# Optimization experiments

Measured on AMD Instinct MI355X. Metric: run time of the kernel, lower is better.

The kernel has to match this reference:

```python
import jax, jax.numpy as jnp
import numpy as np

N, E, D, H, OUT, L, AH = 50000, 800000, 128, 128, 2, 4, 16
LN_EPS = 1e-5


def setup_inputs() -> dict:
    key = jax.random.key(0)
    ks = jax.random.split(key, 8)
    s = lambda k, shape, scale: jax.random.normal(k, shape, jnp.float32) * scale
    return {
        "node_features": jax.random.normal(ks[0], (N, D), jnp.float32),
        "edge_index": jax.random.randint(ks[1], (2, E), 0, N),
        "W_self": s(ks[2], (L, D, H), 0.05),
        "b_self": jnp.zeros((L, H), jnp.float32),
        "W_ctx": s(ks[3], (L, 2 * D, H), 0.05),
        "b_ctx": jnp.zeros((L, H), jnp.float32),
        "att_W1": s(ks[4], (L, H, AH), 0.1),
        "att_b1": jnp.zeros((L, AH), jnp.float32),
        "att_w2": s(ks[5], (L, AH), 0.1),
        "ln_gamma": jnp.ones((L, H), jnp.float32),
        "ln_beta": jnp.zeros((L, H), jnp.float32),
        "fusion_logits": jnp.ones((L,), jnp.float32),
        "cls_W": s(ks[6], (H, OUT), 0.05),
        "cls_b": jnp.zeros((OUT,), jnp.float32),
    }


def _aggregate(x, src, tgt, n):
    # PyG add-aggregation of message cat([x_i - x_j, x_j]) at target nodes.
    # sum_over_edges(x_tgt - x_src) at tgt == deg(tgt)*x[tgt] - sum x_src, so we
    # avoid materializing the [E, 2D] edge tensor.
    ones = jnp.ones((src.shape[0],), x.dtype)
    deg = jax.ops.segment_sum(ones, tgt, num_segments=n)          # [N]
    agg_j = jax.ops.segment_sum(x[src], tgt, num_segments=n)      # [N, D]
    return jnp.concatenate([deg[:, None] * x - agg_j, agg_j], -1)  # [N, 2D]


def _layer_norm(x, gamma, beta):
    mu = x.mean(axis=-1, keepdims=True)
    var = ((x - mu) ** 2).mean(axis=-1, keepdims=True)
    return (x - mu) * jax.lax.rsqrt(var + LN_EPS) * gamma + beta


def _conv(x, src, tgt, Ws, bs, Wc, bc, A1, a1b, a2):
    n = x.shape[0]
    self_view = x @ Ws + bs                              # [N, H]
    out_view = _aggregate(x, src, tgt, n) @ Wc + bc      # outgoing (edge_index)
    in_view = _aggregate(x, tgt, src, n) @ Wc + bc       # incoming (reversed)
    mv = jnp.stack([self_view, out_view, in_view], axis=1)  # [N, 3, H]
    scores = jnp.einsum('nvh,ha->nva', jnp.tanh(jnp.einsum('nvh,ha->nva', mv, A1) + a1b), a2[:, None])[..., 0]
    w = jax.nn.softmax(scores, axis=1)                    # softmax over 3 views
    return jnp.einsum('nv,nvh->nh', w, mv)


def reference(node_features, edge_index, W_self, b_self, W_ctx, b_ctx,
              att_W1, att_b1, att_w2, ln_gamma, ln_beta,
              fusion_logits, cls_W, cls_b):
    src, tgt = edge_index[0], edge_index[1]
    x = node_features
    layer_outputs = []
    for l in range(L):
        h = _conv(x, src, tgt, W_self[l], b_self[l], W_ctx[l], b_ctx[l],
                  att_W1[l], att_b1[l], att_w2[l])
        h = jax.nn.relu(_layer_norm(h, ln_gamma[l], ln_beta[l]))
        # dropout is identity in eval mode
        x = h + x if l > 0 else h
        layer_outputs.append(x)
    fw = jax.nn.softmax(fusion_logits)
    fused = sum(fw[i] * layer_outputs[i] for i in range(L))
    return fused @ cls_W + cls_b
```

## Files before the change

### kernel.cpp

```cpp
#include <hip/hip_runtime.h>

#define N_NODES 50000
#define N_EDGES 800000
#define DD 128
#define HH 128
#define LL 4
#define AHH 16
#define LN_EPS 1e-5f
#define NCOLS 432
#define SCAN_B 512
#define SCAN_NB ((N_NODES + SCAN_B - 1) / SCAN_B)
#define WTPAD 136
#define WT_BLOCKS ((LL*NCOLS*DD)/256)
#define NBKT 196
#define BKT_CAP 8192
#define CVT_BLOCKS ((N_NODES*DD + 255)/256)
#define BKT_BLOCKS ((N_EDGES + 2047)/2048)

typedef unsigned short u16;
typedef unsigned int u32;
typedef __attribute__((ext_vector_type(8))) short short8;
typedef __attribute__((ext_vector_type(4))) float f32x4;

__device__ __forceinline__ float bf2f(u16 h){
  u32 u = ((u32)h) << 16;
  return __builtin_bit_cast(float, u);
}
__device__ __forceinline__ float bflo(u32 v){ return __builtin_bit_cast(float, v << 16); }
__device__ __forceinline__ float bfhi(u32 v){ return __builtin_bit_cast(float, v & 0xffff0000u); }
__device__ __forceinline__ u16 f2bf(float x){
  u32 u = __builtin_bit_cast(u32, x);
  u += 0x7fffu + ((u >> 16) & 1u);
  return (u16)(u >> 16);
}

__global__ void k_fail(float* out){
  int i = blockIdx.x*256 + threadIdx.x;
  if (i < N_NODES*2) out[i] = 1.0e6f;
}

__global__ __launch_bounds__(256) void k_cvt_hist_bkt(const float* __restrict__ X,
    u16* __restrict__ Xb, const int* __restrict__ ei, int* degO, int* degI,
    int* gcur, u32* __restrict__ bktO, u32* __restrict__ bktI){
  if (blockIdx.x < CVT_BLOCKS){
    int i = blockIdx.x*256 + threadIdx.x;
    if (i < N_NODES*DD) Xb[i] = f2bf(X[i]);
    if (i < N_EDGES){
      atomicAdd(&degO[ei[N_EDGES + i]], 1);
      atomicAdd(&degI[ei[i]], 1);
    }
    return;
  }
  __shared__ int histO[NBKT], histI[NBKT], baseO[NBKT], baseI[NBKT];
  int tid = threadIdx.x;
  int e0 = (blockIdx.x - CVT_BLOCKS)*2048;
  if (tid < NBKT){ histO[tid] = 0; histI[tid] = 0; }
  __syncthreads();
  int s[8], t[8];
  #pragma unroll
  for (int k = 0; k < 8; ++k){
    int e = e0 + k*256 + tid;
    bool ok = e < N_EDGES;
    s[k] = ok ? ei[e] : -1;
    t[k] = ok ? ei[N_EDGES + e] : -1;
    if (ok){
      atomicAdd(&histO[t[k] >> 8], 1);
      atomicAdd(&histI[s[k] >> 8], 1);
    }
  }
  __syncthreads();
  if (tid < NBKT){
    baseO[tid] = atomicAdd(&gcur[tid],        histO[tid]);
    baseI[tid] = atomicAdd(&gcur[NBKT + tid], histI[tid]);
  }
  __syncthreads();
  if (tid < NBKT){ histO[tid] = 0; histI[tid] = 0; }
  __syncthreads();
  #pragma unroll
  for (int k = 0; k < 8; ++k){
    if (s[k] >= 0){
      int bO = t[k] >> 8, bI = s[k] >> 8;
      int rO = atomicAdd(&histO[bO], 1);
      int rI = atomicAdd(&histI[bI], 1);
      u32 iO = (u32)bO*BKT_CAP + (u32)(baseO[bO] + rO);
      u32 iI = (u32)bI*BKT_CAP + (u32)(baseI[bI] + rI);
      if (iO >= (u32)NBKT*BKT_CAP) iO = (u32)NBKT*BKT_CAP - 1;
      if (iI >= (u32)NBKT*BKT_CAP) iI = (u32)NBKT*BKT_CAP - 1;
      bktO[iO] = ((u32)(t[k] & 255) << 16) | (u32)s[k];
      bktI[iI] = ((u32)(s[k] & 255) << 16) | (u32)t[k];
    }
  }
}

__global__ __launch_bounds__(SCAN_B) void k_scan1(const int* __restrict__ degO,
                                                  const int* __restrict__ degI, int* bsum){
  int b = blockIdx.x, t = threadIdx.x;
  const int* deg = blockIdx.y ? degI : degO;
  int i = b*SCAN_B + t;
  int v = (i < N_NODES) ? deg[i] : 0;
  #pragma unroll
  for (int m = 1; m < 64; m <<= 1) v += __shfl_xor(v, m);
  __shared__ int ws[SCAN_B/64];
  if ((t & 63) == 0) ws[t >> 6] = v;
  __syncthreads();
  if (t == 0){
    int s = 0;
    for (int w = 0; w < SCAN_B/64; ++w) s += ws[w];
    bsum[blockIdx.y*SCAN_NB + b] = s;
  }
}
__global__ void k_scan2(int* bsum, int* offO, int* offI){
  if (threadIdx.x == 0){
    int run = 0;
    for (int i = 0; i < SCAN_NB; ++i){ int v = bsum[i]; bsum[i] = run; run += v; }
    offO[N_NODES] = run;
    run = 0;
    for (int i = 0; i < SCAN_NB; ++i){ int v = bsum[SCAN_NB+i]; bsum[SCAN_NB+i] = run; run += v; }
    offI[N_NODES] = run;
  }
}
__global__ __launch_bounds__(SCAN_B) void k_scan3(const int* __restrict__ degO,
                                                  const int* __restrict__ degI,
                                                  const int* __restrict__ bsum,
                                                  int* offO, int* offI){
  int b = blockIdx.x, t = threadIdx.x, lane = t & 63, w = t >> 6;
  const int* deg = blockIdx.y ? degI : degO;
  int* off = blockIdx.y ? offI : offO;
  int i = b*SCAN_B + t;
  int v = (i < N_NODES) ? deg[i] : 0;
  int x = v;
  #pragma unroll
  for (int m = 1; m < 64; m <<= 1){ int tt = __shfl_up(x, m); if (lane >= m) x += tt; }
  __shared__ int ws[SCAN_B/64];
  if (lane == 63) ws[w] = x;
  __syncthreads();
  int woff = 0;
  for (int k = 0; k < w; ++k) woff += ws[k];
  if (i < N_NODES) off[i] = bsum[blockIdx.y*SCAN_NB + b] + woff + x - v;
}

__global__ __launch_bounds__(256) void k_packsort(const float* __restrict__ Wself,
                       const float* __restrict__ Wctx,
                       const float* __restrict__ A1, const float* __restrict__ bs,
                       const float* __restrict__ bc, u16* __restrict__ WT,
                       float* bsA, float* bcA,
                       const u32* __restrict__ bktO, const u32* __restrict__ bktI,
                       const int* __restrict__ offO, const int* __restrict__ offI,
                       int* __restrict__ csrO, int* __restrict__ csrI){
  if (blockIdx.x > WT_BLOCKS){
    int sb = blockIdx.x - (WT_BLOCKS + 1);
    int d = sb >= NBKT;
    int b = d ? sb - NBKT : sb;
    const u32* bkt = d ? bktI : bktO;
    const int* off = d ? offI : offO;
    int* csr = d ? csrI : csrO;
    __shared__ int hist[256], pref[256], cur[256], wsum[4];
    int tid = threadIdx.x;
    int lo = b*256, hi = min(lo + 256, N_NODES);
    int gbase = off[lo];
    int cnt = off[hi] - gbase;
    if (cnt > BKT_CAP) cnt = BKT_CAP;
    hist[tid] = 0; cur[tid] = 0;
    __syncthreads();
    const u32* bb = bkt + (size_t)b*BKT_CAP;
    for (int i = tid; i < cnt; i += 256) atomicAdd(&hist[bb[i] >> 16], 1);
    __syncthreads();
    {
      int lane = tid & 63, wid = tid >> 6;
      int h = hist[tid], v = h;
      #pragma unroll
      for (int m = 1; m < 64; m <<= 1){ int tt = __shfl_up(v, m); if (lane >= m) v += tt; }
      if (lane == 63) wsum[wid] = v;
      __syncthreads();
      int add = 0;
      for (int w = 0; w < wid; ++w) add += wsum[w];
      pref[tid] = add + v - h;
    }
    __syncthreads();
    for (int i = tid; i < cnt; i += 256){
      u32 ent = bb[i];
      int loc = (int)(ent >> 16);
      int pos = pref[loc] + atomicAdd(&cur[loc], 1);
      csr[gbase + pos] = (int)(ent & 0xffffu);
    }
    return;
  }
  if (blockIdx.x == WT_BLOCKS){
    int i = threadIdx.x;
    if (i < LL*2*AHH){
      int l = i >> 5, which = (i >> 4) & 1, a = i & 15;
      const float* b = which ? (bc + l*HH) : (bs + l*HH);
      const float* A = A1 + (size_t)l*HH*AHH;
      float v = 0.f;
      for (int h = 0; h < HH; ++h) v += b[h] * A[h*AHH + a];
      (which ? bcA : bsA)[l*AHH + a] = v;
    }
    return;
  }
  int idx = blockIdx.x*256 + threadIdx.x;
  int k = idx & 127;
  int j = (idx >> 7) % NCOLS;
  int l = idx / (NCOLS*DD);
  const float* Ws = Wself + (size_t)l*DD*HH;
  const float* Wc = Wctx + (size_t)l*2*DD*HH;
  const float* A  = A1 + (size_t)l*HH*AHH;
  float v = 0.f;
  if (j < 128) v = Ws[k*HH + j];
  else if (j < 256) v = Wc[k*HH + (j-128)];
  else if (j < 384) v = Wc[(128+k)*HH + (j-256)] - Wc[k*HH + (j-256)];
  else if (j < 400){ int a = j-384; for (int h=0; h<HH; ++h) v += Ws[k*HH+h] * A[h*AHH+a]; }
  else if (j < 416){ int a = j-400; for (int h=0; h<HH; ++h) v += Wc[k*HH+h] * A[h*AHH+a]; }
  else { int a = j-416; for (int h=0; h<HH; ++h) v += (Wc[(128+k)*HH+h] - Wc[k*HH+h]) * A[h*AHH+a]; }
  WT[((size_t)l*NCOLS + j)*DD + k] = f2bf(v);
}

struct GemmOut { u16 *S, *P1, *Pd, *SA, *P1A, *PdA; };

__global__ __launch_bounds__(256) void k_gemm(const u16* __restrict__ X,
                                              const u16* __restrict__ WT, GemmOut o){
  __shared__ u16 lw[3*16*WTPAD];
  int tid = threadIdx.x;
  int wid = tid >> 6, lane = tid & 63;
  int m0 = (blockIdx.x*4 + wid)*16;
  bool mvalid = (m0 < N_NODES);
  int m0c = mvalid ? m0 : (N_NODES - 16);
  int l15 = lane & 15, quad = lane >> 4;
  int sr = tid >> 4, sp = tid & 15;

  f32x4 acc[27];
  #pragma unroll
  for (int j = 0; j < 27; ++j) acc[j] = (f32x4){0.f,0.f,0.f,0.f};

  const u16* xr = X + (size_t)(m0c + l15)*DD + quad*8;
  short8 a[4];
  #pragma unroll
  for (int ks = 0; ks < 4; ++ks) a[ks] = *(const short8*)(xr + ks*32);

  short8 st[3];
  #pragma unroll
  for (int k = 0; k < 3; ++k)
    st[k] = *(const short8*)(WT + ((size_t)k*16 + sr)*DD + sp*8);

  for (int stage = 0; stage < 9; ++stage){
    int jbase = stage*3;
    __syncthreads();
    #pragma unroll
    for (int k = 0; k < 3; ++k)
      *(short8*)(&lw[(k*16 + sr)*WTPAD + sp*8]) = st[k];
    __syncthreads();
    if (stage < 8){
      #pragma unroll
      for (int k = 0; k < 3; ++k)
        st[k] = *(const short8*)(WT + ((size_t)(jbase+3+k)*16 + sr)*DD + sp*8);
    }
    #pragma unroll
    for (int k = 0; k < 3; ++k){
      const u16* wb = &lw[(k*16 + l15)*WTPAD + quad*8];
      #pragma unroll
      for (int ks = 0; ks < 4; ++ks){
        short8 b = *(const short8*)(wb + ks*32);
        acc[jbase+k] = __builtin_amdgcn_mfma_f32_16x16x32_bf16(a[ks], b, acc[jbase+k], 0, 0, 0);
      }
    }
  }
  if (!mvalid) return;
  #pragma unroll
  for (int j = 0; j < 27; ++j){
    int col = j*16 + l15;
    #pragma unroll
    for (int r = 0; r < 4; ++r){
      int row = m0 + quad*4 + r;
      u16 hv = f2bf(acc[j][r]);
      if (col < 128)      o.S  [(size_t)row*128 + col]        = hv;
      else if (col < 256) o.P1 [(size_t)row*128 + col - 128]  = hv;
      else if (col < 384) o.Pd [(size_t)row*128 + col - 256]  = hv;
      else if (col < 400) o.SA [(size_t)row*16  + col - 384]  = hv;
      else if (col < 416) o.P1A[(size_t)row*16  + col - 400]  = hv;
      else                o.PdA[(size_t)row*16  + col - 416]  = hv;
    }
  }
}

__global__ __launch_bounds__(256) void k_aggepi(int l,
  const u16* __restrict__ S, const u16* __restrict__ P1,
  const u16* __restrict__ Pd, const u16* __restrict__ PdA,
  const u16* __restrict__ SA, const u16* __restrict__ P1A,
  const int* __restrict__ offO, const int* __restrict__ offI,
  const int* __restrict__ csrO, const int* __restrict__ csrI,
  const float* __restrict__ b_self, const float* __restrict__ b_ctx,
  const float* __restrict__ bsA, const float* __restrict__ bcA,
  const float* __restrict__ att_b1, const float* __restrict__ att_w2,
  const float* __restrict__ gamma, const float* __restrict__ beta,
  const float* __restrict__ flog,
  u16* __restrict__ xb16,
  const float* __restrict__ clsW, const float* __restrict__ clsB,
  float* __restrict__ out)
{
  __shared__ float red[4][288];
  int tid = threadIdx.x;
  int n = (blockIdx.x * 256 + tid) >> 6;
  int wid = tid >> 6;
  int lane = tid & 63;
  int q = lane & 15, g = lane >> 4;
  const u16* PdQ  = Pd  + (q << 3);
  const u16* PdAQ = PdA + ((lane & 7) << 1);

  int begO = offO[n], endO = offO[n+1];
  int begI = offI[n], endI = offI[n+1];

  float aO[8] = {0.f,0.f,0.f,0.f,0.f,0.f,0.f,0.f};
  float aI[8] = {0.f,0.f,0.f,0.f,0.f,0.f,0.f,0.f};
  float oa0 = 0.f, oa1 = 0.f, ia0 = 0.f, ia1 = 0.f;

  int eO = begO, eI = begI;

#define GATH(csr, e, ACC, p0, p1) { \
    int r_ = (csr)[(e) + g]; \
    uint4 v_ = *(const uint4*)(PdQ + (((u32)r_) << 7)); \
    u32 pa_ = *(const u32*)(PdAQ + (((u32)r_) << 4)); \
    ACC[0] += bflo(v_.x); ACC[1] += bfhi(v_.x); \
    ACC[2] += bflo(v_.y); ACC[3] += bfhi(v_.y); \
    ACC[4] += bflo(v_.z); ACC[5] += bfhi(v_.z); \
    ACC[6] += bflo(v_.w); ACC[7] += bfhi(v_.w); \
    p0 += bflo(pa_); p1 += bfhi(pa_); }

#define GATHM(csr, e, end, ACC, p0, p1) { \
    int e_ = (e) + g; \
    bool ok_ = e_ < (end); \
    int r_ = (csr)[ok_ ? e_ : (end)-1]; \
    uint4 v_ = *(const uint4*)(PdQ + (((u32)r_) << 7)); \
    u32 pa_ = *(const u32*)(PdAQ + (((u32)r_) << 4)); \
    if (!ok_){ v_.x = 0u; v_.y = 0u; v_.z = 0u; v_.w = 0u; pa_ = 0u; } \
    ACC[0] += bflo(v_.x); ACC[1] += bfhi(v_.x); \
    ACC[2] += bflo(v_.y); ACC[3] += bfhi(v_.y); \
    ACC[4] += bflo(v_.z); ACC[5] += bfhi(v_.z); \
    ACC[6] += bflo(v_.w); ACC[7] += bfhi(v_.w); \
    p0 += bflo(pa_); p1 += bfhi(pa_); }

  for (; eO + 4 <= endO && eI + 4 <= endI; eO += 4, eI += 4){
    GATH(csrO, eO, aO, oa0, oa1);
    GATH(csrI, eI, aI, ia0, ia1);
  }
  for (; eO + 4 <= endO; eO += 4) GATH(csrO, eO, aO, oa0, oa1);
  for (; eI + 4 <= endI; eI += 4) GATH(csrI, eI, aI, ia0, ia1);
  if (eO < endO) GATHM(csrO, eO, endO, aO, oa0, oa1);
  if (eI < endI) GATHM(csrI, eI, endI, aI, ia0, ia1);

#undef GATH
#undef GATHM

  #pragma unroll
  for (int j = 0; j < 8; ++j){
    aO[j] += __shfl_xor(aO[j], 16); aO[j] += __shfl_xor(aO[j], 32);
    aI[j] += __shfl_xor(aI[j], 16); aI[j] += __shfl_xor(aI[j], 32);
  }
  oa0 += __shfl_xor(oa0, 16); oa0 += __shfl_xor(oa0, 32);
  oa1 += __shfl_xor(oa1, 16); oa1 += __shfl_xor(oa1, 32);
  ia0 += __shfl_xor(ia0, 16); ia0 += __shfl_xor(ia0, 32);
  ia1 += __shfl_xor(ia1, 16); ia1 += __shfl_xor(ia1, 32);

  if (g == 0){
    #pragma unroll
    for (int j = 0; j < 8; ++j){
      red[wid][q*8 + j]       = aO[j];
      red[wid][128 + q*8 + j] = aI[j];
    }
    if (q < 8){
      red[wid][256 + q*2]     = oa0;
      red[wid][256 + q*2 + 1] = oa1;
      red[wid][272 + q*2]     = ia0;
      red[wid][272 + q*2 + 1] = ia1;
    }
  }
  int f0 = lane * 2;
  int a16 = lane & 15;
  float ao0 = red[wid][f0],       ao1 = red[wid][f0 + 1];
  float ai0 = red[wid][128 + f0], ai1 = red[wid][128 + f0 + 1];
  float aoa = red[wid][256 + a16];
  float aia = red[wid][272 + a16];

  float dO = (float)(endO - begO), dI = (float)(endI - begI);

  u32 sv = *(const u32*)(S  + (size_t)n*128 + f0);
  u32 pv = *(const u32*)(P1 + (size_t)n*128 + f0);
  float2 bsv = *(const float2*)(b_self + l*128 + f0);
  float2 bcv = *(const float2*)(b_ctx  + l*128 + f0);
  float p10 = bflo(pv), p11 = bfhi(pv);
  float mv00 = bflo(sv) + bsv.x;
  float mv01 = bfhi(sv) + bsv.y;
  float mv10 = dO*p10 + ao0 + bcv.x, mv11 = dO*p11 + ao1 + bcv.y;
  float mv20 = dI*p10 + ai0 + bcv.x, mv21 = dI*p11 + ai1 + bcv.y;

  int a = a16, v = g;
  float u = 0.f;
  if (v < 3){
    float t;
    if (v == 0)      t = bf2f(SA[(size_t)n*16 + a]) + bsA[l*16 + a];
    else if (v == 1) t = dO*bf2f(P1A[(size_t)n*16 + a]) + aoa + bcA[l*16 + a];
    else             t = dI*bf2f(P1A[(size_t)n*16 + a]) + aia + bcA[l*16 + a];
    u = tanhf(t + att_b1[l*16 + a]) * att_w2[l*16 + a];
  }
  u += __shfl_xor(u, 1); u += __shfl_xor(u, 2);
  u += __shfl_xor(u, 4); u += __shfl_xor(u, 8);
  float s0 = __shfl(u, 0), s1 = __shfl(u, 16), s2 = __shfl(u, 32);
  float mx = fmaxf(s0, fmaxf(s1, s2));
  float e0 = __expf(s0-mx), e1 = __expf(s1-mx), e2 = __expf(s2-mx);
  float inv = 1.f / (e0 + e1 + e2);
  float w0 = e0*inv, w1 = e1*inv, w2v = e2*inv;
  float h0 = w0*mv00 + w1*mv10 + w2v*mv20;
  float h1 = w0*mv01 + w1*mv11 + w2v*mv21;

  float sum = h0 + h1, sq = h0*h0 + h1*h1;
  #pragma unroll
  for (int m = 1; m < 64; m <<= 1){ sum += __shfl_xor(sum, m); sq += __shfl_xor(sq, m); }
  float mu = sum * (1.f/128.f);
  float var = sq * (1.f/128.f) - mu*mu;
  float rs = rsqrtf(var + LN_EPS);
  float2 gv = *(const float2*)(gamma + l*128 + f0);
  float2 bv = *(const float2*)(beta  + l*128 + f0);
  float y0 = fmaxf((h0 - mu)*rs*gv.x + bv.x, 0.f);
  float y1 = fmaxf((h1 - mu)*rs*gv.y + bv.y, 0.f);
  float xn0 = y0, xn1 = y1;
  if (l > 0){
    u32 xv = *(const u32*)(xb16 + (size_t)n*128 + f0);
    xn0 += bflo(xv); xn1 += bfhi(xv);
  }
  *(u32*)(xb16 + (size_t)n*128 + f0) = (u32)f2bf(xn0) | ((u32)f2bf(xn1) << 16);

  float g0 = flog[0], g1 = flog[1], g2 = flog[2], g3 = flog[3];
  float gm = fmaxf(fmaxf(g0,g1), fmaxf(g2,g3));
  float q0 = __expf(g0-gm), q1 = __expf(g1-gm), q2 = __expf(g2-gm), q3 = __expf(g3-gm);
  float fwl = (l==0?q0 : l==1?q1 : l==2?q2 : q3) / (q0+q1+q2+q3);

  float4 w = *(const float4*)(clsW + lane*4);
  float o0 = xn0*w.x + xn1*w.z;
  float o1 = xn0*w.y + xn1*w.w;
  #pragma unroll
  for (int m = 1; m < 64; m <<= 1){ o0 += __shfl_xor(o0, m); o1 += __shfl_xor(o1, m); }
  if (lane == 0){
    float2* op = (float2*)(out + (size_t)n*2);
    float2 prev = (l > 0) ? *op : make_float2(0.f, 0.f);
    float r0 = prev.x + fwl*o0, r1 = prev.y + fwl*o1;
    if (l == LL-1){ r0 += clsB[0]; r1 += clsB[1]; }
    *op = make_float2(r0, r1);
  }
}

extern "C" void kernel_launch(void* const* d_in, const int* in_sizes, int n_in,
                              void* d_out, int out_size, void* d_ws, size_t ws_size,
                              hipStream_t stream){
  const float* X0    = (const float*)d_in[0];
  const int*   EI    = (const int*)d_in[1];
  const float* Wself = (const float*)d_in[2];
  const float* bs    = (const float*)d_in[3];
  const float* Wctx  = (const float*)d_in[4];
  const float* bc    = (const float*)d_in[5];
  const float* A1    = (const float*)d_in[6];
  const float* ab1   = (const float*)d_in[7];
  const float* aw2   = (const float*)d_in[8];
  const float* gam   = (const float*)d_in[9];
  const float* bet   = (const float*)d_in[10];
  const float* flog  = (const float*)d_in[11];
  const float* clsW  = (const float*)d_in[12];
  const float* clsB  = (const float*)d_in[13];
  float* out = (float*)d_out;

  char* wsp = (char*)d_ws;
  size_t o = 0;
  auto alloc = [&](size_t b)->char*{ char* p = wsp + o; o = (o + b + 255) & ~(size_t)255; return p; };
  u16*  xb16  = (u16*) alloc((size_t)N_NODES*128*2);
  u16*  S     = (u16*) alloc((size_t)N_NODES*128*2);
  u16*  P1    = (u16*) alloc((size_t)N_NODES*128*2);
  u16*  Pdb   = (u16*) alloc((size_t)N_NODES*128*2);
  u16*  PdAb  = (u16*) alloc((size_t)N_NODES*16*2);
  u16*  SAb   = (u16*) alloc((size_t)N_NODES*16*2);
  u16*  P1A   = (u16*) alloc((size_t)N_NODES*16*2);
  u16*  WT    = (u16*) alloc((size_t)LL*NCOLS*128*2);
  float* bsA  = (float*)alloc(LL*16*4);
  float* bcA  = (float*)alloc(LL*16*4);
  int* bsum   = (int*) alloc((size_t)2*SCAN_NB*4);
  int* degO   = (int*) alloc((size_t)N_NODES*4);
  int* degI   = (int*) alloc((size_t)N_NODES*4);
  int* gcur   = (int*) alloc((size_t)2*NBKT*4);
  int* offO   = (int*) alloc((size_t)(N_NODES+1)*4);
  int* offI   = (int*) alloc((size_t)(N_NODES+1)*4);
  int* csrO   = (int*) alloc((size_t)N_EDGES*4);
  int* csrI   = (int*) alloc((size_t)N_EDGES*4);

  if (ws_size < o){
    k_fail<<<(N_NODES*2+255)/256, 256, 0, stream>>>(out);
    return;
  }

  u32* bktO = (u32*)S;
  u32* bktI = (u32*)P1;

  (void)hipMemsetAsync(degO, 0, (size_t)((char*)offO - (char*)degO), stream);

  k_cvt_hist_bkt<<<CVT_BLOCKS + BKT_BLOCKS, 256, 0, stream>>>(X0, xb16, EI, degO, degI,
                                                              gcur, bktO, bktI);
  k_scan1<<<dim3(SCAN_NB,2), SCAN_B, 0, stream>>>(degO, degI, bsum);
  k_scan2<<<1, 64, 0, stream>>>(bsum, offO, offI);
  k_scan3<<<dim3(SCAN_NB,2), SCAN_B, 0, stream>>>(degO, degI, bsum, offO, offI);
  k_packsort<<<WT_BLOCKS + 1 + 2*NBKT, 256, 0, stream>>>(Wself, Wctx, A1, bs, bc, WT, bsA, bcA,
                                                         bktO, bktI, offO, offI, csrO, csrI);

  GemmOut go{S, P1, Pdb, SAb, P1A, PdAb};
  const int gemm_blocks = ((N_NODES/16) + 3) / 4;
  for (int l = 0; l < LL; ++l){
    k_gemm<<<gemm_blocks, 256, 0, stream>>>(xb16, WT + (size_t)l*NCOLS*128, go);
    k_aggepi<<<N_NODES/4, 256, 0, stream>>>(l, S, P1, Pdb, PdAb, SAb, P1A,
                                            offO, offI, csrO, csrI,
                                            bs, bc, bsA, bcA, ab1, aw2,
                                            gam, bet, flog, xb16,
                                            clsW, clsB, out);
  }
}
```

Baseline: 612.9 us.

## Derive node degrees from bucket histograms instead of global atomics

Removes the per-edge global atomic degree counting from the conversion kernel. Degrees are now computed per bucket with shared-memory histograms over the already-bucketed edges. Block sums for the scan come straight from the bucket counters, so the scan1 pass goes away. The memset shrinks to the bucket counters, and bucket blocks are reordered to launch before the conversion blocks. The cost is one extra pass that reads the bucket arrays.

```diff
diff --git a/kernel.cpp b/kernel.cpp
--- a/kernel.cpp
+++ b/kernel.cpp
@@ -39,21 +39,17 @@
   if (i < N_NODES*2) out[i] = 1.0e6f;
 }
 
-__global__ __launch_bounds__(256) void k_cvt_hist_bkt(const float* __restrict__ X,
-    u16* __restrict__ Xb, const int* __restrict__ ei, int* degO, int* degI,
+__global__ __launch_bounds__(256) void k_cvt_bkt(const float* __restrict__ X,
+    u16* __restrict__ Xb, const int* __restrict__ ei,
     int* gcur, u32* __restrict__ bktO, u32* __restrict__ bktI){
-  if (blockIdx.x < CVT_BLOCKS){
-    int i = blockIdx.x*256 + threadIdx.x;
+  if (blockIdx.x >= BKT_BLOCKS){
+    int i = (blockIdx.x - BKT_BLOCKS)*256 + threadIdx.x;
     if (i < N_NODES*DD) Xb[i] = f2bf(X[i]);
-    if (i < N_EDGES){
-      atomicAdd(&degO[ei[N_EDGES + i]], 1);
-      atomicAdd(&degI[ei[i]], 1);
-    }
     return;
   }
   __shared__ int histO[NBKT], histI[NBKT], baseO[NBKT], baseI[NBKT];
   int tid = threadIdx.x;
-  int e0 = (blockIdx.x - CVT_BLOCKS)*2048;
+  int e0 = blockIdx.x*2048;
   if (tid < NBKT){ histO[tid] = 0; histI[tid] = 0; }
   __syncthreads();
   int s[8], t[8];
@@ -92,30 +88,32 @@
   }
 }
 
-__global__ __launch_bounds__(SCAN_B) void k_scan1(const int* __restrict__ degO,
-                                                  const int* __restrict__ degI, int* bsum){
-  int b = blockIdx.x, t = threadIdx.x;
-  const int* deg = blockIdx.y ? degI : degO;
-  int i = b*SCAN_B + t;
-  int v = (i < N_NODES) ? deg[i] : 0;
-  #pragma unroll
-  for (int m = 1; m < 64; m <<= 1) v += __shfl_xor(v, m);
-  __shared__ int ws[SCAN_B/64];
-  if ((t & 63) == 0) ws[t >> 6] = v;
-  __syncthreads();
-  if (t == 0){
-    int s = 0;
-    for (int w = 0; w < SCAN_B/64; ++w) s += ws[w];
-    bsum[blockIdx.y*SCAN_NB + b] = s;
-  }
-}
-__global__ void k_scan2(int* bsum, int* offO, int* offI){
+__global__ __launch_bounds__(256) void k_bhist(const int* __restrict__ gcur,
+    const u32* __restrict__ bktO, const u32* __restrict__ bktI,
+    int* __restrict__ degO, int* __restrict__ degI){
+  __shared__ int hist[256];
+  int sb = blockIdx.x;
+  int d = sb >= NBKT;
+  int b = d ? sb - NBKT : sb;
+  const u32* bkt = (d ? bktI : bktO) + (size_t)b*BKT_CAP;
+  int cnt = gcur[d*NBKT + b];
+  if (cnt > BKT_CAP) cnt = BKT_CAP;
+  int tid = threadIdx.x;
+  hist[tid] = 0;
+  __syncthreads();
+  for (int i = tid; i < cnt; i += 256) atomicAdd(&hist[bkt[i] >> 16], 1);
+  __syncthreads();
+  int n = b*256 + tid;
+  if (n < N_NODES) (d ? degI : degO)[n] = hist[tid];
+}
+
+__global__ void k_scan2(const int* __restrict__ gcur, int* bsum, int* offO, int* offI){
   if (threadIdx.x == 0){
     int run = 0;
-    for (int i = 0; i < SCAN_NB; ++i){ int v = bsum[i]; bsum[i] = run; run += v; }
+    for (int i = 0; i < SCAN_NB; ++i){ bsum[i] = run; run += gcur[2*i] + gcur[2*i+1]; }
     offO[N_NODES] = run;
     run = 0;
-    for (int i = 0; i < SCAN_NB; ++i){ int v = bsum[SCAN_NB+i]; bsum[SCAN_NB+i] = run; run += v; }
+    for (int i = 0; i < SCAN_NB; ++i){ bsum[SCAN_NB+i] = run; run += gcur[NBKT+2*i] + gcur[NBKT+2*i+1]; }
     offI[N_NODES] = run;
   }
 }
@@ -495,12 +493,11 @@
   u32* bktO = (u32*)S;
   u32* bktI = (u32*)P1;
 
-  (void)hipMemsetAsync(degO, 0, (size_t)((char*)offO - (char*)degO), stream);
-
-  k_cvt_hist_bkt<<<CVT_BLOCKS + BKT_BLOCKS, 256, 0, stream>>>(X0, xb16, EI, degO, degI,
-                                                              gcur, bktO, bktI);
-  k_scan1<<<dim3(SCAN_NB,2), SCAN_B, 0, stream>>>(degO, degI, bsum);
-  k_scan2<<<1, 64, 0, stream>>>(bsum, offO, offI);
+  (void)hipMemsetAsync(gcur, 0, (size_t)2*NBKT*4, stream);
+
+  k_cvt_bkt<<<BKT_BLOCKS + CVT_BLOCKS, 256, 0, stream>>>(X0, xb16, EI, gcur, bktO, bktI);
+  k_bhist<<<2*NBKT, 256, 0, stream>>>(gcur, bktO, bktI, degO, degI);
+  k_scan2<<<1, 64, 0, stream>>>(gcur, bsum, offO, offI);
   k_scan3<<<dim3(SCAN_NB,2), SCAN_B, 0, stream>>>(degO, degI, bsum, offO, offI);
   k_packsort<<<WT_BLOCKS + 1 + 2*NBKT, 256, 0, stream>>>(Wself, Wctx, A1, bs, bc, WT, bsA, bcA,
                                                          bktO, bktI, offO, offI, csrO, csrI);
```

After: 557.3 us, median of 2. 9.1% less time.
